# Kernel tuning notes

Hardware: AMD Instinct MI355X
Metric: run time of the kernel (lower is better)

The kernel has to match this reference:

```python
import jax, jax.numpy as jnp
import numpy as np

HEAD_SIZE = 64

def setup_inputs() -> dict:
    key = jax.random.key(0)
    ks = jax.random.split(key, 7)
    B, S, H, D = 8, 2048, 768, HEAD_SIZE
    scale = 1.0 / np.sqrt(H)
    return {
        "x": jax.random.normal(ks[0], (B, S, H), dtype=jnp.float32),
        "Wq": jax.random.normal(ks[1], (H, D), dtype=jnp.float32) * scale,
        "bq": jax.random.normal(ks[2], (D,), dtype=jnp.float32) * 0.02,
        "Wk": jax.random.normal(ks[3], (H, D), dtype=jnp.float32) * scale,
        "bk": jax.random.normal(ks[4], (D,), dtype=jnp.float32) * 0.02,
        "Wv": jax.random.normal(ks[5], (H, D), dtype=jnp.float32) * scale,
        "bv": jax.random.normal(ks[6], (D,), dtype=jnp.float32) * 0.02,
    }

def reference(x, Wq, bq, Wk, bk, Wv, bv):
    # Q/K/V projections: [B,S,H] @ [H,D] -> [B,S,D]
    q = x @ Wq + bq
    k = x @ Wk + bk
    v = x @ Wv + bv
    # scaled dot-product scores: [B,S,S]
    scores = jnp.einsum("bsd,btd->bst", q, k) / jnp.sqrt(jnp.float32(HEAD_SIZE))
    probs = jax.nn.softmax(scores, axis=-1)
    # dropout p=0.0 -> identity (matches eval / p=0 training)
    out = jnp.einsum("bst,btd->bsd", probs, v)
    return (out, probs)
```

## Files before the change

### kernel.cpp

```cpp
#include <hip/hip_runtime.h>

#define BB 8
#define SS 2048
#define HH 768
#define DD 64
#define BK 64
#define NK (HH / BK)

typedef short bf16x8 __attribute__((ext_vector_type(8)));
typedef short bf16x4 __attribute__((ext_vector_type(4)));
typedef float f32x16 __attribute__((ext_vector_type(16)));

static __device__ __forceinline__ short f2bf(float f) {
    union { float f; unsigned u; } v; v.f = f;
    unsigned u = v.u + 0x7fff + ((v.u >> 16) & 1);
    return (short)(u >> 16);
}

__global__ __launch_bounds__(256) void w_convert(
    const float* __restrict__ Wq, const float* __restrict__ Wk,
    const float* __restrict__ Wv, short* __restrict__ wT)
{
    __shared__ float ws[64][65];
    const int jj   = blockIdx.x / 12;
    const int h0   = (blockIdx.x % 12) * 64;
    const int tid  = threadIdx.x;
    const float* Wsrc = (jj == 0) ? Wq : (jj == 1 ? Wk : Wv);

    {
        const int hl = tid >> 4;
        const int c4 = tid & 15;
        #pragma unroll
        for (int p = 0; p < 4; ++p) {
            const int h = hl + p * 16;
            float4 v = ((const float4*)(Wsrc + (long)(h0 + h) * DD))[c4];
            ws[h][c4 * 4 + 0] = v.x; ws[h][c4 * 4 + 1] = v.y;
            ws[h][c4 * 4 + 2] = v.z; ws[h][c4 * 4 + 3] = v.w;
        }
    }
    __syncthreads();

    const int d   = tid >> 2;
    const int seg = tid & 3;
    bf16x8 t0, t1;
    #pragma unroll
    for (int m = 0; m < 8; ++m) {
        t0[m] = f2bf(ws[seg * 16 + m][d]);
        t1[m] = f2bf(ws[seg * 16 + 8 + m][d]);
    }
    short* dst = wT + ((long)jj * 64 + d) * HH + h0 + seg * 16;
    *(bf16x8*)dst = t0;
    *(bf16x8*)(dst + 8) = t1;
}

__global__ __launch_bounds__(384) void qkv_mfma(
    const float* __restrict__ x, const short* __restrict__ wT,
    const float* __restrict__ bq, const float* __restrict__ bk,
    const float* __restrict__ bv,
    short* __restrict__ qo, short* __restrict__ ko, short* __restrict__ vT)
{
    __shared__ short xs[2][32][68];

    const int tid  = threadIdx.x;
    const int w    = tid >> 6;
    const int lane = tid & 63;
    const int l31  = lane & 31;
    const int h    = lane >> 5;
    const long row0 = (long)blockIdx.x * 32;

    const int r0 = tid >> 4,        c0 = tid & 15;
    const int r1 = (tid + 384) >> 4, c1 = (tid + 384) & 15;
    const bool has1 = (tid + 384) < 512;

    f32x16 acc;
    #pragma unroll
    for (int i = 0; i < 16; ++i) acc[i] = 0.f;

    float4 st0, st1;
    st0 = ((const float4*)(x + (row0 + r0) * HH))[c0];
    if (has1) st1 = ((const float4*)(x + (row0 + r1) * HH))[c1];
    {
        bf16x4 b0; b0[0]=f2bf(st0.x); b0[1]=f2bf(st0.y); b0[2]=f2bf(st0.z); b0[3]=f2bf(st0.w);
        *(bf16x4*)&xs[0][r0][c0 * 4] = b0;
        if (has1) {
            bf16x4 b1; b1[0]=f2bf(st1.x); b1[1]=f2bf(st1.y); b1[2]=f2bf(st1.z); b1[3]=f2bf(st1.w);
            *(bf16x4*)&xs[0][r1][c1 * 4] = b1;
        }
    }
    __syncthreads();

    const int col = w * 32 + l31;
    const short* wcol = wT + (long)col * HH + h * 8;

    for (int it = 0; it < NK; ++it) {
        const int cur = it & 1;
        if (it < NK - 1) {
            st0 = ((const float4*)(x + (row0 + r0) * HH + (it + 1) * BK))[c0];
            if (has1) st1 = ((const float4*)(x + (row0 + r1) * HH + (it + 1) * BK))[c1];
        }
        #pragma unroll
        for (int kt = 0; kt < 4; ++kt) {
            bf16x8 af = *(const bf16x8*)&xs[cur][l31][kt * 16 + h * 8];
            bf16x8 bf = *(const bf16x8*)(wcol + it * BK + kt * 16);
            acc = __builtin_amdgcn_mfma_f32_32x32x16_bf16(af, bf, acc, 0, 0, 0);
        }
        if (it < NK - 1) {
            __syncthreads();
            bf16x4 b0; b0[0]=f2bf(st0.x); b0[1]=f2bf(st0.y); b0[2]=f2bf(st0.z); b0[3]=f2bf(st0.w);
            *(bf16x4*)&xs[cur ^ 1][r0][c0 * 4] = b0;
            if (has1) {
                bf16x4 b1; b1[0]=f2bf(st1.x); b1[1]=f2bf(st1.y); b1[2]=f2bf(st1.z); b1[3]=f2bf(st1.w);
                *(bf16x4*)&xs[cur ^ 1][r1][c1 * 4] = b1;
            }
            __syncthreads();
        }
    }

    short (*vs)[68] = xs[0];
    const int j = w >> 1;
    const int d = (w & 1) * 32 + l31;
    const float* bptr = (j == 0) ? bq : (j == 1 ? bk : bv);
    const float bias = bptr[d];

    __syncthreads();

    #pragma unroll
    for (int i = 0; i < 16; ++i) {
        const int r = (i & 3) + 8 * (i >> 2) + 4 * h;
        const short val = f2bf(acc[i] + bias);
        if (j == 0)      qo[(row0 + r) * DD + d] = val;
        else if (j == 1) ko[(row0 + r) * DD + d] = val;
        else             vs[r][d] = val;
    }
    __syncthreads();

    if (tid < 256) {
        const int b  = (int)(row0 >> 11);
        const int s0 = (int)(row0 & (SS - 1));
        const int dd  = tid >> 2;
        const int seg = tid & 3;
        bf16x8 t;
        #pragma unroll
        for (int m = 0; m < 8; ++m) t[m] = vs[seg * 8 + m][dd];
        *(bf16x8*)(vT + ((long)b * DD + dd) * SS + s0 + seg * 8) = t;
    }
}

__global__ __launch_bounds__(512) void attn(
    const short* __restrict__ qb, const short* __restrict__ kb,
    const short* __restrict__ vT,
    float* __restrict__ out, float* __restrict__ probs)
{
    __shared__ float maxbuf[32][9];
    __shared__ float sumbuf[32][9];
    __shared__ float obuf[32][65];

    const int tid  = threadIdx.x;
    const int w    = tid >> 6;
    const int lane = tid & 63;
    const int l31  = lane & 31;
    const int h    = lane >> 5;

    const int b    = blockIdx.x & 7;
    const int row0 = (blockIdx.x >> 3) * 32;
    const int wk0  = w * 256;

    for (int i = tid; i < 32 * 65; i += 512) ((float*)obuf)[i] = 0.f;

    bf16x8 qf[4];
    const short* qrow = qb + ((long)(b * SS + row0 + l31)) * DD + h * 8;
    #pragma unroll
    for (int kt = 0; kt < 4; ++kt) qf[kt] = *(const bf16x8*)(qrow + kt * 16);

    f32x16 acc[8];
    const short* kbase = kb + ((long)(b * SS + wk0 + l31)) * DD + h * 8;
    #pragma unroll
    for (int ct = 0; ct < 8; ++ct) {
        f32x16 a;
        #pragma unroll
        for (int i = 0; i < 16; ++i) a[i] = 0.f;
        const short* kp = kbase + (long)ct * 32 * DD;
        #pragma unroll
        for (int kt = 0; kt < 4; ++kt) {
            bf16x8 kf = *(const bf16x8*)(kp + kt * 16);
            a = __builtin_amdgcn_mfma_f32_32x32x16_bf16(kf, qf[kt], a, 0, 0, 0);
        }
        acc[ct] = a;
    }

    float m = -1e30f;
    #pragma unroll
    for (int ct = 0; ct < 8; ++ct)
        #pragma unroll
        for (int i = 0; i < 16; ++i) m = fmaxf(m, acc[ct][i]);
    m = fmaxf(m, __shfl_xor(m, 32));
    if (lane < 32) maxbuf[l31][w] = m;
    __syncthreads();

    float gm = maxbuf[l31][0];
    #pragma unroll
    for (int i = 1; i < 8; ++i) gm = fmaxf(gm, maxbuf[l31][i]);

    float s = 0.f;
    #pragma unroll
    for (int ct = 0; ct < 8; ++ct)
        #pragma unroll
        for (int i = 0; i < 16; ++i) {
            const float e = __expf((acc[ct][i] - gm) * 0.125f);
            acc[ct][i] = e;
            s += e;
        }
    s += __shfl_xor(s, 32);
    if (lane < 32) sumbuf[l31][w] = s;
    __syncthreads();

    float gs = 0.f;
    #pragma unroll
    for (int i = 0; i < 8; ++i) gs += sumbuf[l31][i];
    const float inv = 1.f / gs;

    f32x16 oacc[2];
    #pragma unroll
    for (int i = 0; i < 16; ++i) { oacc[0][i] = 0.f; oacc[1][i] = 0.f; }

    float* prp = probs + ((long)(b * SS + row0 + l31)) * SS + wk0;
    const short* vbase = vT + (long)b * DD * SS + wk0 + h * 8;

    #pragma unroll
    for (int ct = 0; ct < 8; ++ct) {
        unsigned P[4][2];
        #pragma unroll
        for (int j = 0; j < 4; ++j) {
            const float p0 = acc[ct][4 * j + 0] * inv;
            const float p1 = acc[ct][4 * j + 1] * inv;
            const float p2 = acc[ct][4 * j + 2] * inv;
            const float p3 = acc[ct][4 * j + 3] * inv;
            float4 pv = make_float4(p0, p1, p2, p3);
            *(float4*)(prp + ct * 32 + 8 * j + 4 * h) = pv;
            unsigned pj0, pj1;
            asm("v_cvt_pk_bf16_f32 %0, %1, %2" : "=v"(pj0) : "v"(p0), "v"(p1));
            asm("v_cvt_pk_bf16_f32 %0, %1, %2" : "=v"(pj1) : "v"(p2), "v"(p3));
            P[j][0] = pj0; P[j][1] = pj1;
        }
        #pragma unroll
        for (int kk = 0; kk < 2; ++kk) {
            unsigned x0 = P[2 * kk][0], y0 = P[2 * kk + 1][0];
            unsigned x1 = P[2 * kk][1], y1 = P[2 * kk + 1][1];
            asm("v_permlane32_swap_b32 %0, %1" : "+v"(x0), "+v"(y0));
            asm("v_permlane32_swap_b32 %0, %1" : "+v"(x1), "+v"(y1));
            union { unsigned u[4]; bf16x8 v; } pf;
            pf.u[0] = x0; pf.u[1] = x1; pf.u[2] = y0; pf.u[3] = y1;
            #pragma unroll
            for (int nt = 0; nt < 2; ++nt) {
                bf16x8 vf = *(const bf16x8*)(vbase + (long)(nt * 32 + l31) * SS
                                             + ct * 32 + kk * 16);
                oacc[nt] = __builtin_amdgcn_mfma_f32_32x32x16_bf16(vf, pf.v, oacc[nt], 0, 0, 0);
            }
        }
    }

    #pragma unroll
    for (int nt = 0; nt < 2; ++nt)
        #pragma unroll
        for (int i = 0; i < 16; ++i) {
            const int d = nt * 32 + (i & 3) + 8 * (i >> 2) + 4 * h;
            atomicAdd(&obuf[l31][d], oacc[nt][i]);
        }
    __syncthreads();

    const int q   = tid >> 4;
    const int seg = tid & 15;
    float4 val = make_float4(obuf[q][seg * 4 + 0], obuf[q][seg * 4 + 1],
                             obuf[q][seg * 4 + 2], obuf[q][seg * 4 + 3]);
    *(float4*)(out + ((long)(b * SS + row0 + q)) * DD + seg * 4) = val;
}

extern "C" void kernel_launch(void* const* d_in, const int* in_sizes, int n_in,
                              void* d_out, int out_size, void* d_ws, size_t ws_size,
                              hipStream_t stream) {
    const float* x  = (const float*)d_in[0];
    const float* Wq = (const float*)d_in[1];
    const float* bq = (const float*)d_in[2];
    const float* Wk = (const float*)d_in[3];
    const float* bk = (const float*)d_in[4];
    const float* Wv = (const float*)d_in[5];
    const float* bv = (const float*)d_in[6];

    float* out   = (float*)d_out;
    float* probs = (float*)d_out + (long)BB * SS * DD;

    short* q  = (short*)d_ws;
    short* k  = q + (long)BB * SS * DD;
    short* vT = k + (long)BB * SS * DD;
    short* wT = vT + (long)BB * SS * DD;

    w_convert<<<36, 256, 0, stream>>>(Wq, Wk, Wv, wT);
    qkv_mfma<<<(BB * SS) / 32, 384, 0, stream>>>(x, wT, bq, bk, bv, q, k, vT);
    attn<<<BB * (SS / 32), 512, 0, stream>>>(q, k, vT, out, probs);
}
```

Baseline: 134.7 us.

## Split attention into row-sum pass and key-split main pass without max subtraction

Softmax becomes two passes. A first kernel recomputes QK^T and accumulates only exp2-based row sums, with no running max. A second kernel, split across two key halves per row block, recomputes scores, writes normalized probabilities and accumulates the partial output into a zeroed buffer with global atomics. K and V tiles are staged through double-buffered LDS with prefetch instead of being loaded directly per lane. The QK^T work is done twice and out needs a memset plus atomics. Dropping the max subtraction can overflow exp for inputs with large scores.

```diff
diff --git a/kernel.cpp b/kernel.cpp
--- a/kernel.cpp
+++ b/kernel.cpp
@@ -10,11 +10,18 @@
 typedef short bf16x8 __attribute__((ext_vector_type(8)));
 typedef short bf16x4 __attribute__((ext_vector_type(4)));
 typedef float f32x16 __attribute__((ext_vector_type(16)));
+typedef float f32x4 __attribute__((ext_vector_type(4)));
+
+#define EXPC 0.18033688011112042f
 
 static __device__ __forceinline__ short f2bf(float f) {
     union { float f; unsigned u; } v; v.f = f;
     unsigned u = v.u + 0x7fff + ((v.u >> 16) & 1);
     return (short)(u >> 16);
+}
+
+static __device__ __forceinline__ int sigma(int j) {
+    return (j & 19) | ((j & 4) << 1) | ((j & 8) >> 1);
 }
 
 __global__ __launch_bounds__(256) void w_convert(
@@ -146,14 +153,12 @@
     }
 }
 
-__global__ __launch_bounds__(512) void attn(
+__global__ __launch_bounds__(512) void attn_sum(
     const short* __restrict__ qb, const short* __restrict__ kb,
-    const short* __restrict__ vT,
-    float* __restrict__ out, float* __restrict__ probs)
+    float* __restrict__ sums)
 {
-    __shared__ float maxbuf[32][9];
+    __shared__ short kbuf[2][256][68];
     __shared__ float sumbuf[32][9];
-    __shared__ float obuf[32][65];
 
     const int tid  = threadIdx.x;
     const int w    = tid >> 6;
@@ -163,116 +168,183 @@
 
     const int b    = blockIdx.x & 7;
     const int row0 = (blockIdx.x >> 3) * 32;
-    const int wk0  = w * 256;
-
-    for (int i = tid; i < 32 * 65; i += 512) ((float*)obuf)[i] = 0.f;
+    const int srow = sigma(l31);
 
     bf16x8 qf[4];
-    const short* qrow = qb + ((long)(b * SS + row0 + l31)) * DD + h * 8;
+    const short* qrow = qb + ((long)(b * SS) + row0 + l31) * DD + h * 8;
     #pragma unroll
     for (int kt = 0; kt < 4; ++kt) qf[kt] = *(const bf16x8*)(qrow + kt * 16);
 
-    f32x16 acc[8];
-    const short* kbase = kb + ((long)(b * SS + wk0 + l31)) * DD + h * 8;
-    #pragma unroll
-    for (int ct = 0; ct < 8; ++ct) {
+    const int sr = tid >> 3, sc = (tid & 7) * 8;
+    const short* kg = kb + ((long)b * SS) * DD;
+
+    bf16x8 st[4];
+    #pragma unroll
+    for (int p = 0; p < 4; ++p)
+        st[p] = *(const bf16x8*)(kg + ((long)(p * 64 + sr)) * DD + sc);
+    #pragma unroll
+    for (int p = 0; p < 4; ++p)
+        *(bf16x8*)&kbuf[0][p * 64 + sr][sc] = st[p];
+    __syncthreads();
+
+    float s = 0.f;
+    for (int c = 0; c < 8; ++c) {
+        if (c < 7) {
+            #pragma unroll
+            for (int p = 0; p < 4; ++p)
+                st[p] = *(const bf16x8*)(kg + ((long)((c + 1) * 256 + p * 64 + sr)) * DD + sc);
+        }
         f32x16 a;
         #pragma unroll
         for (int i = 0; i < 16; ++i) a[i] = 0.f;
-        const short* kp = kbase + (long)ct * 32 * DD;
         #pragma unroll
         for (int kt = 0; kt < 4; ++kt) {
-            bf16x8 kf = *(const bf16x8*)(kp + kt * 16);
+            bf16x8 kf = *(const bf16x8*)&kbuf[c & 1][w * 32 + srow][kt * 16 + h * 8];
             a = __builtin_amdgcn_mfma_f32_32x32x16_bf16(kf, qf[kt], a, 0, 0, 0);
         }
-        acc[ct] = a;
-    }
-
-    float m = -1e30f;
-    #pragma unroll
-    for (int ct = 0; ct < 8; ++ct)
-        #pragma unroll
-        for (int i = 0; i < 16; ++i) m = fmaxf(m, acc[ct][i]);
-    m = fmaxf(m, __shfl_xor(m, 32));
-    if (lane < 32) maxbuf[l31][w] = m;
-    __syncthreads();
-
-    float gm = maxbuf[l31][0];
-    #pragma unroll
-    for (int i = 1; i < 8; ++i) gm = fmaxf(gm, maxbuf[l31][i]);
-
-    float s = 0.f;
-    #pragma unroll
-    for (int ct = 0; ct < 8; ++ct)
-        #pragma unroll
-        for (int i = 0; i < 16; ++i) {
-            const float e = __expf((acc[ct][i] - gm) * 0.125f);
-            acc[ct][i] = e;
-            s += e;
-        }
+        #pragma unroll
+        for (int r = 0; r < 16; ++r) s += __builtin_amdgcn_exp2f(a[r] * EXPC);
+        if (c < 7) {
+            #pragma unroll
+            for (int p = 0; p < 4; ++p)
+                *(bf16x8*)&kbuf[(c + 1) & 1][p * 64 + sr][sc] = st[p];
+        }
+        __syncthreads();
+    }
+
     s += __shfl_xor(s, 32);
     if (lane < 32) sumbuf[l31][w] = s;
     __syncthreads();
-
-    float gs = 0.f;
-    #pragma unroll
-    for (int i = 0; i < 8; ++i) gs += sumbuf[l31][i];
-    const float inv = 1.f / gs;
+    if (tid < 32) {
+        float gs = 0.f;
+        #pragma unroll
+        for (int i = 0; i < 8; ++i) gs += sumbuf[tid][i];
+        sums[(long)b * SS + row0 + tid] = gs;
+    }
+}
+
+__global__ __launch_bounds__(512) void attn_main(
+    const short* __restrict__ qb, const short* __restrict__ kb,
+    const short* __restrict__ vT, const float* __restrict__ sums,
+    float* __restrict__ out, float* __restrict__ probs)
+{
+    __shared__ short kbuf[256][68];
+    __shared__ short vbuf[64][260];
+    __shared__ float obuf[32][65];
+
+    const int tid  = threadIdx.x;
+    const int w    = tid >> 6;
+    const int lane = tid & 63;
+    const int l31  = lane & 31;
+    const int h    = lane >> 5;
+
+    const int b    = blockIdx.x & 7;
+    const int idx  = blockIdx.x >> 3;
+    const int row0 = (idx & 63) * 32;
+    const int kh   = idx >> 6;
+    const int k0   = kh * 1024;
+    const int srow = sigma(l31);
+
+    for (int i = tid; i < 32 * 65; i += 512) ((float*)obuf)[i] = 0.f;
+
+    bf16x8 qf[4];
+    const short* qrow = qb + ((long)(b * SS) + row0 + l31) * DD + h * 8;
+    #pragma unroll
+    for (int kt = 0; kt < 4; ++kt) qf[kt] = *(const bf16x8*)(qrow + kt * 16);
+
+    const float inv = 1.f / sums[(long)b * SS + row0 + l31];
 
     f32x16 oacc[2];
     #pragma unroll
     for (int i = 0; i < 16; ++i) { oacc[0][i] = 0.f; oacc[1][i] = 0.f; }
 
-    float* prp = probs + ((long)(b * SS + row0 + l31)) * SS + wk0;
-    const short* vbase = vT + (long)b * DD * SS + wk0 + h * 8;
-
-    #pragma unroll
-    for (int ct = 0; ct < 8; ++ct) {
-        unsigned P[4][2];
-        #pragma unroll
-        for (int j = 0; j < 4; ++j) {
-            const float p0 = acc[ct][4 * j + 0] * inv;
-            const float p1 = acc[ct][4 * j + 1] * inv;
-            const float p2 = acc[ct][4 * j + 2] * inv;
-            const float p3 = acc[ct][4 * j + 3] * inv;
-            float4 pv = make_float4(p0, p1, p2, p3);
-            *(float4*)(prp + ct * 32 + 8 * j + 4 * h) = pv;
-            unsigned pj0, pj1;
-            asm("v_cvt_pk_bf16_f32 %0, %1, %2" : "=v"(pj0) : "v"(p0), "v"(p1));
-            asm("v_cvt_pk_bf16_f32 %0, %1, %2" : "=v"(pj1) : "v"(p2), "v"(p3));
-            P[j][0] = pj0; P[j][1] = pj1;
-        }
+    const int sr = tid >> 3, sc = (tid & 7) * 8;
+    const int vr = tid >> 5, vc = (tid & 31) * 8;
+    const short* kg = kb + ((long)(b * SS) + k0) * DD;
+    const short* vg = vT + (long)b * DD * SS + k0;
+
+    bf16x8 st[4], sv[4];
+    #pragma unroll
+    for (int p = 0; p < 4; ++p) {
+        st[p] = *(const bf16x8*)(kg + ((long)(p * 64 + sr)) * DD + sc);
+        sv[p] = *(const bf16x8*)(vg + ((long)(p * 16 + vr)) * SS + vc);
+    }
+    #pragma unroll
+    for (int p = 0; p < 4; ++p) {
+        *(bf16x8*)&kbuf[p * 64 + sr][sc] = st[p];
+        *(bf16x8*)&vbuf[p * 16 + vr][vc] = sv[p];
+    }
+    __syncthreads();
+
+    for (int c = 0; c < 4; ++c) {
+        if (c < 3) {
+            #pragma unroll
+            for (int p = 0; p < 4; ++p) {
+                st[p] = *(const bf16x8*)(kg + ((long)((c + 1) * 256 + p * 64 + sr)) * DD + sc);
+                sv[p] = *(const bf16x8*)(vg + ((long)(p * 16 + vr)) * SS + (c + 1) * 256 + vc);
+            }
+        }
+        f32x16 a;
+        #pragma unroll
+        for (int i = 0; i < 16; ++i) a[i] = 0.f;
+        #pragma unroll
+        for (int kt = 0; kt < 4; ++kt) {
+            bf16x8 kf = *(const bf16x8*)&kbuf[w * 32 + srow][kt * 16 + h * 8];
+            a = __builtin_amdgcn_mfma_f32_32x32x16_bf16(kf, qf[kt], a, 0, 0, 0);
+        }
+        #pragma unroll
+        for (int r = 0; r < 16; ++r) a[r] = __builtin_amdgcn_exp2f(a[r] * EXPC);
+
+        float* pp = probs + ((long)(b * SS) + row0 + l31) * SS + k0 + c * 256 + w * 32 + 8 * h;
         #pragma unroll
         for (int kk = 0; kk < 2; ++kk) {
-            unsigned x0 = P[2 * kk][0], y0 = P[2 * kk + 1][0];
-            unsigned x1 = P[2 * kk][1], y1 = P[2 * kk + 1][1];
-            asm("v_permlane32_swap_b32 %0, %1" : "+v"(x0), "+v"(y0));
-            asm("v_permlane32_swap_b32 %0, %1" : "+v"(x1), "+v"(y1));
             union { unsigned u[4]; bf16x8 v; } pf;
-            pf.u[0] = x0; pf.u[1] = x1; pf.u[2] = y0; pf.u[3] = y1;
+            #pragma unroll
+            for (int i = 0; i < 4; ++i) {
+                unsigned u;
+                asm("v_cvt_pk_bf16_f32 %0, %1, %2"
+                    : "=v"(u) : "v"(a[8 * kk + 2 * i]), "v"(a[8 * kk + 2 * i + 1]));
+                pf.u[i] = u;
+            }
             #pragma unroll
             for (int nt = 0; nt < 2; ++nt) {
-                bf16x8 vf = *(const bf16x8*)(vbase + (long)(nt * 32 + l31) * SS
-                                             + ct * 32 + kk * 16);
+                bf16x8 vf = *(const bf16x8*)&vbuf[nt * 32 + l31][w * 32 + kk * 16 + h * 8];
                 oacc[nt] = __builtin_amdgcn_mfma_f32_32x32x16_bf16(vf, pf.v, oacc[nt], 0, 0, 0);
             }
+            f32x4 o0, o1;
+            o0[0] = a[8 * kk + 0] * inv; o0[1] = a[8 * kk + 1] * inv;
+            o0[2] = a[8 * kk + 2] * inv; o0[3] = a[8 * kk + 3] * inv;
+            o1[0] = a[8 * kk + 4] * inv; o1[1] = a[8 * kk + 5] * inv;
+            o1[2] = a[8 * kk + 6] * inv; o1[3] = a[8 * kk + 7] * inv;
+            *(f32x4*)(pp + kk * 16)     = o0;
+            *(f32x4*)(pp + kk * 16 + 4) = o1;
+        }
+        if (c < 3) {
+            __syncthreads();
+            #pragma unroll
+            for (int p = 0; p < 4; ++p) {
+                *(bf16x8*)&kbuf[p * 64 + sr][sc] = st[p];
+                *(bf16x8*)&vbuf[p * 16 + vr][vc] = sv[p];
+            }
+            __syncthreads();
         }
     }
 
     #pragma unroll
     for (int nt = 0; nt < 2; ++nt)
         #pragma unroll
-        for (int i = 0; i < 16; ++i) {
-            const int d = nt * 32 + (i & 3) + 8 * (i >> 2) + 4 * h;
-            atomicAdd(&obuf[l31][d], oacc[nt][i]);
-        }
-    __syncthreads();
-
-    const int q   = tid >> 4;
-    const int seg = tid & 15;
-    float4 val = make_float4(obuf[q][seg * 4 + 0], obuf[q][seg * 4 + 1],
-                             obuf[q][seg * 4 + 2], obuf[q][seg * 4 + 3]);
-    *(float4*)(out + ((long)(b * SS + row0 + q)) * DD + seg * 4) = val;
+        for (int i = 0; i < 16; ++i)
+            atomicAdd(&obuf[l31][nt * 32 + (i & 3) + 8 * (i >> 2) + 4 * h],
+                      oacc[nt][i] * inv);
+    __syncthreads();
+
+    {
+        const int q  = tid >> 4;
+        const int c4 = tid & 15;
+        float* op = out + ((long)(b * SS) + row0 + q) * DD + c4 * 4;
+        #pragma unroll
+        for (int j = 0; j < 4; ++j) atomicAdd(op + j, obuf[q][c4 * 4 + j]);
+    }
 }
 
 extern "C" void kernel_launch(void* const* d_in, const int* in_sizes, int n_in,
@@ -289,12 +361,15 @@
     float* out   = (float*)d_out;
     float* probs = (float*)d_out + (long)BB * SS * DD;
 
-    short* q  = (short*)d_ws;
-    short* k  = q + (long)BB * SS * DD;
-    short* vT = k + (long)BB * SS * DD;
-    short* wT = vT + (long)BB * SS * DD;
+    short* q    = (short*)d_ws;
+    short* k    = q + (long)BB * SS * DD;
+    short* vT   = k + (long)BB * SS * DD;
+    short* wT   = vT + (long)BB * SS * DD;
+    float* sums = (float*)((char*)d_ws + (8u << 20));
 
     w_convert<<<36, 256, 0, stream>>>(Wq, Wk, Wv, wT);
-    qkv_mfma<<<(BB * SS) / 32, 384, 0, stream>>>(x, wT, bq, bk, bv, q, k, vT);
-    attn<<<BB * (SS / 32), 512, 0, stream>>>(q, k, vT, out, probs);
-}
+    qkv_mfma<<<(BB * SS) / 32, 384, 0, stream>>>(x, Wq ? wT : wT, bq, bk, bv, q, k, vT);
+    hipMemsetAsync(out, 0, (size_t)BB * SS * DD * sizeof(float), stream);
+    attn_sum<<<BB * (SS / 32), 512, 0, stream>>>(q, k, sums);
+    attn_main<<<BB * (SS / 32) * 2, 512, 0, stream>>>(q, k, vT, sums, out, probs);
+}
```

After: 193.6 us (median of 4 runs). 43.8% more time.
